# Performance work log

Measured on AMD Instinct MI355X. Metric: run time of the kernel, lower is better.

## Reference

```python
import jax, jax.numpy as jnp
import numpy as np

NUM_BANDS = 30
SPLIT_FREQ = 30
M_PARAM = 1
DIM = 2048
BATCH = 16384


def _dct_mat(N):
    # Orthonormal DCT-II matrix D: dct(x) = x @ D.T, idct(y) = y @ D
    n = np.arange(N, dtype=np.float64)
    kk = n[:, None]
    M = np.cos(np.pi * (n + 0.5) * kk / N)
    s = np.full(N, np.sqrt(2.0 / N))
    s[0] = np.sqrt(1.0 / N)
    return jnp.asarray((M * s[:, None]).astype(np.float32))


def _band_scale(freq_weights, k, N):
    # Precompute the per-frequency scale vector the torch loop applies band-by-band.
    pts = np.linspace(0, N - 1, NUM_BANDS + 1).astype(np.int64)  # torch .long() truncation
    scale = jnp.ones((N,), dtype=freq_weights.dtype)
    for i in range(NUM_BANDS):
        s, e = int(pts[i]), int(pts[i + 1])
        if e <= SPLIT_FREQ:
            f = 1.0 + freq_weights[i] * k * (1.0 - i / NUM_BANDS)
        else:
            f = 1.0 - freq_weights[i] * k * (1.0 - (i - NUM_BANDS // M_PARAM) / NUM_BANDS)
        scale = scale.at[s:e].set(f)  # bands are disjoint; base is 1
    return scale


def setup_inputs() -> dict:
    key = jax.random.key(0)
    ks = jax.random.split(key, 6)
    g = 0.02  # small init like xavier_uniform with gain 0.5
    return {
        "x": jax.random.normal(ks[0], (BATCH, DIM), dtype=jnp.float32),
        "freq_weights": jnp.ones((NUM_BANDS,), dtype=jnp.float32),
        "k": jnp.float32(0.3),
        "W1": jax.random.normal(ks[1], (1024, DIM), dtype=jnp.float32) * g,
        "b1": jnp.zeros((1024,), dtype=jnp.float32),
        "W2": jax.random.normal(ks[2], (512, 1024), dtype=jnp.float32) * g,
        "b2": jnp.zeros((512,), dtype=jnp.float32),
        "Wmu": jax.random.normal(ks[3], (256, 512), dtype=jnp.float32) * g,
        "bmu": jnp.zeros((256,), dtype=jnp.float32),
        "Wlv": jax.random.normal(ks[4], (256, 512), dtype=jnp.float32) * g,
        "blv": jnp.zeros((256,), dtype=jnp.float32),
    }


def reference(x, freq_weights, k, W1, b1, W2, b2, Wmu, bmu, Wlv, blv):
    N = x.shape[-1]
    D = _dct_mat(N)
    # DCT -> per-band reweight -> IDCT, fused as two matmuls and one vector multiply
    xd = (x @ D.T) * _band_scale(freq_weights, k, N)
    xe = xd @ D
    h = jax.nn.relu(xe @ W1.T + b1)
    h = jax.nn.relu(h @ W2.T + b2)
    mu = h @ Wmu.T + bmu
    logvar = h @ Wlv.T + blv
    return (mu, logvar)
```

## Files before the change

### kernel.cpp

```cpp
#include <hip/hip_runtime.h>
#include <hip/hip_bf16.h>
#include <math.h>

#define DIM 2048
#define BATCH 16384

typedef __attribute__((ext_vector_type(8))) short short8;
typedef __attribute__((ext_vector_type(4))) short short4v;
typedef __attribute__((ext_vector_type(4))) float floatx4;
typedef unsigned short ushort_t;

__device__ __forceinline__ ushort_t f2bf(float f) {
    union { float f; unsigned u; } v; v.f = f;
    unsigned r = v.u + 0x7FFFu + ((v.u >> 16) & 1u);
    return (ushort_t)(r >> 16);
}

__global__ void k_scale(const float* __restrict__ fw, const float* __restrict__ kp,
                        float* __restrict__ s) {
    int n = blockIdx.x * blockDim.x + threadIdx.x;
    if (n >= DIM) return;
    float kv = kp[0];
    float f = 1.0f;
    for (int i = 0; i < 30; ++i) {
        long s0 = (long)((double)i       * (double)(DIM - 1) / 30.0);
        long e0 = (long)((double)(i + 1) * (double)(DIM - 1) / 30.0);
        if (n >= s0 && n < e0) {
            if (e0 <= 30)
                f = 1.0f + fw[i] * kv * (1.0f - (float)i / 30.0f);
            else
                f = 1.0f - fw[i] * kv * (1.0f - (float)(i - 30) / 30.0f);
        }
    }
    s[n] = f;
}

__global__ void k_gen_d(ushort_t* __restrict__ D, ushort_t* __restrict__ Dt) {
    int idx = blockIdx.x * blockDim.x + threadIdx.x;
    int r = idx >> 11;
    int c = idx & (DIM - 1);
    const float w  = 7.6699039394282058e-4f;
    const float s0 = 0.02209708691207961f;
    const float s1 = 0.03125f;
    int m1 = ((2 * c + 1) * r) & (4 * DIM - 1);
    int m2 = ((2 * r + 1) * c) & (4 * DIM - 1);
    float v1 = __cosf(w * (float)m1) * (r == 0 ? s0 : s1);
    float v2 = __cosf(w * (float)m2) * (c == 0 ? s0 : s1);
    D[idx]  = f2bf(v1);
    Dt[idx] = f2bf(v2);
}

#define U_W1   262144
#define U_W2    65536
#define U_WH    16384
__global__ void k_cast_w(const float* __restrict__ W1, const float* __restrict__ W2,
                         const float* __restrict__ Wmu, const float* __restrict__ Wlv,
                         ushort_t* __restrict__ W1bf, ushort_t* __restrict__ W2bf,
                         ushort_t* __restrict__ Wcat) {
    int i = blockIdx.x * blockDim.x + threadIdx.x;
    const float* src; ushort_t* dst; int u;
    if (i < U_W1)                    { src = W1;  dst = W1bf;             u = i; }
    else if (i < U_W1 + U_W2)        { src = W2;  dst = W2bf;             u = i - U_W1; }
    else if (i < U_W1 + U_W2 + U_WH) { src = Wmu; dst = Wcat;             u = i - U_W1 - U_W2; }
    else                             { src = Wlv; dst = Wcat + 8 * U_WH;  u = i - U_W1 - U_W2 - U_WH; }
    const float4* p = reinterpret_cast<const float4*>(src) + 2 * (size_t)u;
    float4 a = p[0], b = p[1];
    short8 r;
    r[0] = (short)f2bf(a.x); r[1] = (short)f2bf(a.y);
    r[2] = (short)f2bf(a.z); r[3] = (short)f2bf(a.w);
    r[4] = (short)f2bf(b.x); r[5] = (short)f2bf(b.y);
    r[6] = (short)f2bf(b.z); r[7] = (short)f2bf(b.w);
    *reinterpret_cast<short8*>(dst + 8 * (size_t)u) = r;
}

__global__ void k_cast_x(const float* __restrict__ in, ushort_t* __restrict__ out) {
    int i = blockIdx.x * blockDim.x + threadIdx.x;
    const float4* p = reinterpret_cast<const float4*>(in) + 2 * (size_t)i;
    float4 a = p[0], b = p[1];
    short8 r;
    r[0] = (short)f2bf(a.x); r[1] = (short)f2bf(a.y);
    r[2] = (short)f2bf(a.z); r[3] = (short)f2bf(a.w);
    r[4] = (short)f2bf(b.x); r[5] = (short)f2bf(b.y);
    r[6] = (short)f2bf(b.z); r[7] = (short)f2bf(b.w);
    *reinterpret_cast<short8*>(out + 8 * (size_t)i) = r;
}

__global__ void k_red(const float* __restrict__ P, ushort_t* __restrict__ out,
                      const float* __restrict__ scale, int n4, int n4row) {
    int i = blockIdx.x * blockDim.x + threadIdx.x;
    const float4* p = reinterpret_cast<const float4*>(P);
    float4 a = p[i], b = p[i + n4], c = p[i + 2 * n4], d = p[i + 3 * n4];
    float4 s;
    s.x = a.x + b.x + c.x + d.x;
    s.y = a.y + b.y + c.y + d.y;
    s.z = a.z + b.z + c.z + d.z;
    s.w = a.w + b.w + c.w + d.w;
    if (scale) {
        float4 sc = reinterpret_cast<const float4*>(scale)[i & (n4row - 1)];
        s.x *= sc.x; s.y *= sc.y; s.z *= sc.z; s.w *= sc.w;
    }
    short4v o;
    o[0] = (short)f2bf(s.x); o[1] = (short)f2bf(s.y);
    o[2] = (short)f2bf(s.z); o[3] = (short)f2bf(s.w);
    *reinterpret_cast<short4v*>(out + 4 * (size_t)i) = o;
}

template<int TM, int TN, int BK, int EPI, bool SK4>
__device__ __forceinline__ void gemm_core(
        const ushort_t* __restrict__ A, const ushort_t* __restrict__ B,
        ushort_t* __restrict__ Cb, float* __restrict__ Cf,
        const float* __restrict__ ep0, const float* __restrict__ ep1,
        int M, int N, int K, int KC) {
    constexpr int BM = 32 * TM;
    constexpr int BN = 32 * TN;
    constexpr int SEGS = BK / 8;
    constexpr int RSH  = (BK == 32) ? 1 : 0;
    constexpr int SSH  = (SEGS == 4) ? 2 : 3;
    __shared__ __align__(16) ushort_t As[BM * BK];
    __shared__ __align__(16) ushort_t Bs[BN * BK];

    const int tid  = threadIdx.x;
    const int lane = tid & 63;
    const int wave = tid >> 6;
    const int wm   = wave >> 1;
    const int wn   = wave & 1;
    const int q    = lane >> 4;
    const int l16  = lane & 15;

    const int tilesM = M / BM;
    const int tilesN = N / BN;
    int bid = (int)blockIdx.x;
    int sk = 0;
    if constexpr (SK4) { int nt = tilesM * tilesN; sk = bid / nt; bid = bid % nt; }
    const int xcd = bid & 7;
    const int j   = bid >> 3;
    const int bm  = xcd * (tilesM >> 3) + j / tilesN;
    const int bn  = j % tilesN;

    floatx4 acc[TM][TN];
    #pragma unroll
    for (int i = 0; i < TM; ++i)
        #pragma unroll
        for (int jj = 0; jj < TN; ++jj)
            acc[i][jj] = (floatx4){0.f, 0.f, 0.f, 0.f};

    const long aBase = (long)bm * BM * K + (long)sk * KC;
    const long bBase = (long)bn * BN * K + (long)sk * KC;
    const int  KLOOP = SK4 ? KC : K;

    for (int kt = 0; kt < KLOOP; kt += BK) {
        __syncthreads();
        #pragma unroll
        for (int i = 0; i < BM * BK / 2048; ++i) {
            int idx = tid + i * 256;
            int row = idx >> SSH, seg = idx & (SEGS - 1);
            int gseg = seg ^ ((row >> RSH) & (SEGS - 1));
            const ushort_t* g = A + aBase + (long)row * K + kt + gseg * 8;
            __builtin_amdgcn_global_load_lds(
                (const __attribute__((address_space(1))) void*)g,
                (__attribute__((address_space(3))) void*)(As + idx * 8),
                16, 0, 0);
        }
        #pragma unroll
        for (int i = 0; i < BN * BK / 2048; ++i) {
            int idx = tid + i * 256;
            int row = idx >> SSH, seg = idx & (SEGS - 1);
            int gseg = seg ^ ((row >> RSH) & (SEGS - 1));
            const ushort_t* g = B + bBase + (long)row * K + kt + gseg * 8;
            __builtin_amdgcn_global_load_lds(
                (const __attribute__((address_space(1))) void*)g,
                (__attribute__((address_space(3))) void*)(Bs + idx * 8),
                16, 0, 0);
        }
        __syncthreads();

        #pragma unroll
        for (int ks = 0; ks < BK / 32; ++ks) {
            short8 af[TM], bfr[TN];
            #pragma unroll
            for (int t = 0; t < TM; ++t) {
                int srow = wm * TM * 16 + t * 16 + l16;
                int rseg = (ks * 4 + q) ^ ((srow >> RSH) & (SEGS - 1));
                af[t] = *reinterpret_cast<const short8*>(&As[srow * BK + rseg * 8]);
            }
            #pragma unroll
            for (int t = 0; t < TN; ++t) {
                int srow = wn * TN * 16 + t * 16 + l16;
                int rseg = (ks * 4 + q) ^ ((srow >> RSH) & (SEGS - 1));
                bfr[t] = *reinterpret_cast<const short8*>(&Bs[srow * BK + rseg * 8]);
            }
            #pragma unroll
            for (int i = 0; i < TM; ++i)
                #pragma unroll
                for (int jj = 0; jj < TN; ++jj)
                    acc[i][jj] = __builtin_amdgcn_mfma_f32_16x16x32_bf16(
                        af[i], bfr[jj], acc[i][jj], 0, 0, 0);
        }
    }

    #pragma unroll
    for (int i = 0; i < TM; ++i) {
        #pragma unroll
        for (int jj = 0; jj < TN; ++jj) {
            #pragma unroll
            for (int r = 0; r < 4; ++r) {
                int row = bm * BM + wm * TM * 16 + i * 16 + q * 4 + r;
                int col = bn * BN + wn * TN * 16 + jj * 16 + l16;
                float v = acc[i][jj][r];
                if constexpr (EPI == 0) {
                    Cb[(long)row * N + col] = f2bf(v * ep0[col]);
                } else if constexpr (EPI == 1) {
                    Cb[(long)row * N + col] = f2bf(v);
                } else if constexpr (EPI == 2) {
                    v += ep0[col];
                    v = v > 0.f ? v : 0.f;
                    Cb[(long)row * N + col] = f2bf(v);
                } else if constexpr (EPI == 3) {
                    const int half = N >> 1;
                    if (col < half)
                        Cf[(long)row * half + col] = v + ep0[col];
                    else
                        Cf[(long)M * half + (long)row * half + (col - half)] = v + ep1[col - half];
                } else {
                    Cf[(long)sk * M * N + (long)row * N + col] = v;
                }
            }
        }
    }
}

__global__ __launch_bounds__(256) void g0p_sk(const ushort_t* A, const ushort_t* B,
        float* P, int M, int N, int K, int KC) {
    gemm_core<4, 4, 32, 4, true>(A, B, nullptr, P, nullptr, nullptr, M, N, K, KC);
}
__global__ __launch_bounds__(256) void g1p_sk(const ushort_t* A, const ushort_t* B,
        float* P, int M, int N, int K, int KC) {
    gemm_core<4, 4, 32, 4, true>(A, B, nullptr, P, nullptr, nullptr, M, N, K, KC);
}
__global__ __launch_bounds__(256) void g2_xm1(const ushort_t* A, const ushort_t* B,
        ushort_t* Cb, const float* ep0, int M, int N, int K) {
    gemm_core<4, 4, 64, 2, false>(A, B, Cb, nullptr, ep0, nullptr, M, N, K, 0);
}
__global__ __launch_bounds__(256) void g3_h2(const ushort_t* A, const ushort_t* B,
        ushort_t* Cb, const float* ep0, int M, int N, int K) {
    gemm_core<4, 4, 32, 2, false>(A, B, Cb, nullptr, ep0, nullptr, M, N, K, 0);
}
__global__ __launch_bounds__(256) void g4_head(const ushort_t* A, const ushort_t* B,
        float* Cf, const float* ep0, const float* ep1, int M, int N, int K) {
    gemm_core<4, 4, 32, 3, false>(A, B, nullptr, Cf, ep0, ep1, M, N, K, 0);
}

extern "C" void kernel_launch(void* const* d_in, const int* in_sizes, int n_in,
                              void* d_out, int out_size, void* d_ws, size_t ws_size,
                              hipStream_t stream) {
    const float* x   = (const float*)d_in[0];
    const float* fw  = (const float*)d_in[1];
    const float* kp  = (const float*)d_in[2];
    const float* W1  = (const float*)d_in[3];
    const float* b1  = (const float*)d_in[4];
    const float* W2  = (const float*)d_in[5];
    const float* b2  = (const float*)d_in[6];
    const float* Wmu = (const float*)d_in[7];
    const float* bmu = (const float*)d_in[8];
    const float* Wlv = (const float*)d_in[9];
    const float* blv = (const float*)d_in[10];
    float* out = (float*)d_out;

    char* ws = (char*)d_ws;
    const size_t MB = 1024 * 1024;
    ushort_t* W1bf = (ushort_t*)(ws + 0);
    ushort_t* Dbf  = (ushort_t*)(ws + 4   * MB);
    ushort_t* Dtbf = (ushort_t*)(ws + 12  * MB);
    ushort_t* T1sT = (ushort_t*)(ws + 20  * MB);
    ushort_t* H1   = (ushort_t*)(ws + 0);
    float*    P    = (float*)   (ws + 32  * MB);
    ushort_t* Xbf  = (ushort_t*)(ws + 32  * MB);
    ushort_t* H2   = (ushort_t*)(ws + 96  * MB);
    ushort_t* M1T  = (ushort_t*)(ws + 112 * MB);
    ushort_t* W2bf = (ushort_t*)(ws + 116 * MB);
    ushort_t* Wcat = (ushort_t*)(ws + 117 * MB);
    float*    svec = (float*)   (ws + 118 * MB);

    hipLaunchKernelGGL(k_scale, dim3(DIM / 256), dim3(256), 0, stream, fw, kp, svec);
    hipLaunchKernelGGL(k_gen_d, dim3(DIM * DIM / 256), dim3(256), 0, stream, Dbf, Dtbf);
    hipLaunchKernelGGL(k_cast_w, dim3((U_W1 + U_W2 + 2 * U_WH) / 256), dim3(256), 0, stream,
                       W1, W2, Wmu, Wlv, W1bf, W2bf, Wcat);

    hipLaunchKernelGGL(g0p_sk, dim3(8 * 16 * 4), dim3(256), 0, stream,
                       W1bf, Dbf, P, 1024, 2048, 2048, 512);
    hipLaunchKernelGGL(k_red, dim3(1024 * 2048 / 4 / 256), dim3(256), 0, stream,
                       P, T1sT, svec, 1024 * 2048 / 4, 2048 / 4);
    hipLaunchKernelGGL(g1p_sk, dim3(8 * 16 * 4), dim3(256), 0, stream,
                       T1sT, Dtbf, P, 1024, 2048, 2048, 512);
    hipLaunchKernelGGL(k_red, dim3(1024 * 2048 / 4 / 256), dim3(256), 0, stream,
                       P, M1T, nullptr, 1024 * 2048 / 4, 2048 / 4);

    hipLaunchKernelGGL(k_cast_x, dim3(BATCH * DIM / 8 / 256), dim3(256), 0, stream, x, Xbf);

    hipLaunchKernelGGL(g2_xm1, dim3((BATCH / 128) * (1024 / 128)), dim3(256), 0, stream,
                       Xbf, M1T, H1, b1, BATCH, 1024, 2048);
    hipLaunchKernelGGL(g3_h2, dim3((BATCH / 128) * (512 / 128)), dim3(256), 0, stream,
                       H1, W2bf, H2, b2, BATCH, 512, 1024);
    hipLaunchKernelGGL(g4_head, dim3((BATCH / 128) * (512 / 128)), dim3(256), 0, stream,
                       H2, Wcat, out, bmu, blv, BATCH, 512, 512);

    (void)in_sizes; (void)n_in; (void)out_size; (void)ws_size;
}
```

Baseline: 407.7 us.

## Replace main X·M1 GEMM with 256x256 four-stage LDS-pipelined MFMA kernel

Replaces the largest GEMM (16384x1024x2048) with a dedicated kernel using 256x256 tiles, 512 threads, a 4-slot shared-memory ring filled by direct global-to-LDS loads, XOR-swizzled layout, and interleaved barriers with setprio around MFMA bursts. It also remaps block indices so each XCD works on a contiguous band of rows, to improve L2 reuse. The aim is more arithmetic intensity per tile and hiding of global load latency, traded against large LDS use (128 KB per block) and a high register count that may limit occupancy, plus hand-tuned waitcnt logic that is easy to get wrong.

Result: faster. 397.0 us (-2.6%).

```diff
diff --git a/kernel.cpp b/kernel.cpp
--- a/kernel.cpp
+++ b/kernel.cpp
@@ -229,6 +229,157 @@
     }
 }
 
+__global__ __launch_bounds__(512, 2) void g2_256(const ushort_t* __restrict__ A,
+        const ushort_t* __restrict__ B, ushort_t* __restrict__ Cb,
+        const float* __restrict__ bias, int M, int N, int K) {
+    constexpr int BM = 256, BN = 256, BK = 32;
+    __shared__ __align__(16) ushort_t As[4][BM * BK];
+    __shared__ __align__(16) ushort_t Bs[4][BN * BK];
+
+    const int tid  = threadIdx.x;
+    const int lane = tid & 63;
+    const int wave = tid >> 6;
+    const int wm   = wave >> 2;
+    const int wn   = wave & 3;
+    const int q    = lane >> 4;
+    const int l16  = lane & 15;
+
+    const int tilesM = M / BM;
+    const int tilesN = N / BN;
+    int bid = (int)blockIdx.x;
+    const int xcd = bid & 7;
+    const int jb  = bid >> 3;
+    const int bm  = xcd * (tilesM >> 3) + jb / tilesN;
+    const int bn  = jb % tilesN;
+    const int NT  = K / BK;
+
+    const long aBase = (long)bm * BM * K;
+    const long bBase = (long)bn * BN * K;
+
+    floatx4 acc[8][4];
+    #pragma unroll
+    for (int i = 0; i < 8; ++i)
+        #pragma unroll
+        for (int j = 0; j < 4; ++j)
+            acc[i][j] = (floatx4){0.f, 0.f, 0.f, 0.f};
+
+#define STAGE_A(t) do { int _sl = (t) & 3;                                          \
+        _Pragma("unroll")                                                           \
+        for (int _g = 0; _g < 2; ++_g) {                                            \
+            int _idx = _g * 512 + tid;                                              \
+            int _row = _idx >> 2, _seg = _idx & 3;                                  \
+            int _gs = _seg ^ ((_row >> 1) & 3);                                     \
+            const ushort_t* _gp = A + aBase + (long)_row * K + (t) * BK + _gs * 8;  \
+            __builtin_amdgcn_global_load_lds(                                       \
+                (const __attribute__((address_space(1))) void*)_gp,                 \
+                (__attribute__((address_space(3))) void*)(&As[_sl][_idx * 8]),      \
+                16, 0, 0);                                                          \
+        } } while (0)
+#define STAGE_B(t) do { int _sl = (t) & 3;                                          \
+        _Pragma("unroll")                                                           \
+        for (int _g = 0; _g < 2; ++_g) {                                            \
+            int _idx = _g * 512 + tid;                                              \
+            int _row = _idx >> 2, _seg = _idx & 3;                                  \
+            int _gs = _seg ^ ((_row >> 1) & 3);                                     \
+            const ushort_t* _gp = B + bBase + (long)_row * K + (t) * BK + _gs * 8;  \
+            __builtin_amdgcn_global_load_lds(                                       \
+                (const __attribute__((address_space(1))) void*)_gp,                 \
+                (__attribute__((address_space(3))) void*)(&Bs[_sl][_idx * 8]),      \
+                16, 0, 0);                                                          \
+        } } while (0)
+
+    STAGE_A(0); STAGE_B(0);
+    STAGE_A(1); STAGE_B(1);
+    STAGE_A(2); STAGE_B(2);
+    asm volatile("s_waitcnt vmcnt(8)" ::: "memory");
+    __builtin_amdgcn_s_barrier();
+    asm volatile("" ::: "memory");
+
+#define KTILE(tt, DOSTAGE, WAITOP) do {                                             \
+        const int _slot = (tt) & 3;                                                 \
+        short8 bfrag[4], afrag[4];                                                  \
+        _Pragma("unroll")                                                           \
+        for (int _j = 0; _j < 4; ++_j) {                                            \
+            int _sr = wn * 64 + _j * 16 + l16;                                      \
+            int _rs = q ^ ((_sr >> 1) & 3);                                         \
+            bfrag[_j] = *reinterpret_cast<const short8*>(&Bs[_slot][_sr * BK + _rs * 8]); \
+        }                                                                           \
+        _Pragma("unroll")                                                           \
+        for (int _i = 0; _i < 4; ++_i) {                                            \
+            int _sr = wm * 128 + _i * 16 + l16;                                     \
+            int _rs = q ^ ((_sr >> 1) & 3);                                         \
+            afrag[_i] = *reinterpret_cast<const short8*>(&As[_slot][_sr * BK + _rs * 8]); \
+        }                                                                           \
+        if (DOSTAGE) STAGE_A((tt) + 3);                                             \
+        __builtin_amdgcn_s_barrier();                                               \
+        asm volatile("s_waitcnt lgkmcnt(0)" ::: "memory");                          \
+        __builtin_amdgcn_sched_barrier(0);                                          \
+        __builtin_amdgcn_s_setprio(1);                                              \
+        _Pragma("unroll")                                                           \
+        for (int _i = 0; _i < 4; ++_i)                                              \
+            _Pragma("unroll")                                                       \
+            for (int _j = 0; _j < 4; ++_j)                                          \
+                acc[_i][_j] = __builtin_amdgcn_mfma_f32_16x16x32_bf16(              \
+                    afrag[_i], bfrag[_j], acc[_i][_j], 0, 0, 0);                    \
+        __builtin_amdgcn_s_setprio(0);                                              \
+        __builtin_amdgcn_s_barrier();                                               \
+        asm volatile("" ::: "memory");                                              \
+        short8 afrag2[4];                                                           \
+        _Pragma("unroll")                                                           \
+        for (int _i = 0; _i < 4; ++_i) {                                            \
+            int _sr = wm * 128 + 64 + _i * 16 + l16;                                \
+            int _rs = q ^ ((_sr >> 1) & 3);                                         \
+            afrag2[_i] = *reinterpret_cast<const short8*>(&As[_slot][_sr * BK + _rs * 8]); \
+        }                                                                           \
+        if (DOSTAGE) STAGE_B((tt) + 3);                                             \
+        __builtin_amdgcn_s_barrier();                                               \
+        asm volatile("s_waitcnt lgkmcnt(0)" ::: "memory");                          \
+        __builtin_amdgcn_sched_barrier(0);                                          \
+        __builtin_amdgcn_s_setprio(1);                                              \
+        _Pragma("unroll")                                                           \
+        for (int _i = 0; _i < 4; ++_i)                                              \
+            _Pragma("unroll")                                                       \
+            for (int _j = 0; _j < 4; ++_j)                                          \
+                acc[4 + _i][_j] = __builtin_amdgcn_mfma_f32_16x16x32_bf16(          \
+                    afrag2[_i], bfrag[_j], acc[4 + _i][_j], 0, 0, 0);               \
+        __builtin_amdgcn_s_setprio(0);                                              \
+        WAITOP;                                                                     \
+        __builtin_amdgcn_s_barrier();                                               \
+        asm volatile("" ::: "memory");                                              \
+    } while (0)
+
+    int t = 0;
+    for (; t < NT - 3; ++t) {
+        KTILE(t, true, asm volatile("s_waitcnt vmcnt(8)" ::: "memory"));
+    }
+    KTILE(t, false, asm volatile("s_waitcnt vmcnt(4)" ::: "memory")); ++t;
+    KTILE(t, false, asm volatile("s_waitcnt vmcnt(0)" ::: "memory")); ++t;
+    KTILE(t, false, (void)0);
+
+#undef KTILE
+#undef STAGE_A
+#undef STAGE_B
+
+    float bsv[4];
+    #pragma unroll
+    for (int j = 0; j < 4; ++j)
+        bsv[j] = bias[bn * BN + wn * 64 + j * 16 + l16];
+    #pragma unroll
+    for (int i = 0; i < 8; ++i) {
+        int row = bm * BM + wm * 128 + i * 16 + q * 4;
+        #pragma unroll
+        for (int j = 0; j < 4; ++j) {
+            int col = bn * BN + wn * 64 + j * 16 + l16;
+            #pragma unroll
+            for (int r = 0; r < 4; ++r) {
+                float v = acc[i][j][r] + bsv[j];
+                v = v > 0.f ? v : 0.f;
+                Cb[(long)(row + r) * N + col] = f2bf(v);
+            }
+        }
+    }
+}
+
 __global__ __launch_bounds__(256) void g0p_sk(const ushort_t* A, const ushort_t* B,
         float* P, int M, int N, int K, int KC) {
     gemm_core<4, 4, 32, 4, true>(A, B, nullptr, P, nullptr, nullptr, M, N, K, KC);
@@ -236,10 +387,6 @@
 __global__ __launch_bounds__(256) void g1p_sk(const ushort_t* A, const ushort_t* B,
         float* P, int M, int N, int K, int KC) {
     gemm_core<4, 4, 32, 4, true>(A, B, nullptr, P, nullptr, nullptr, M, N, K, KC);
-}
-__global__ __launch_bounds__(256) void g2_xm1(const ushort_t* A, const ushort_t* B,
-        ushort_t* Cb, const float* ep0, int M, int N, int K) {
-    gemm_core<4, 4, 64, 2, false>(A, B, Cb, nullptr, ep0, nullptr, M, N, K, 0);
 }
 __global__ __launch_bounds__(256) void g3_h2(const ushort_t* A, const ushort_t* B,
         ushort_t* Cb, const float* ep0, int M, int N, int K) {
@@ -297,7 +444,7 @@
 
     hipLaunchKernelGGL(k_cast_x, dim3(BATCH * DIM / 8 / 256), dim3(256), 0, stream, x, Xbf);
 
-    hipLaunchKernelGGL(g2_xm1, dim3((BATCH / 128) * (1024 / 128)), dim3(256), 0, stream,
+    hipLaunchKernelGGL(g2_256, dim3((BATCH / 256) * (1024 / 256)), dim3(512), 0, stream,
                        Xbf, M1T, H1, b1, BATCH, 1024, 2048);
     hipLaunchKernelGGL(g3_h2, dim3((BATCH / 128) * (512 / 128)), dim3(256), 0, stream,
                        H1, W2bf, H2, b2, BATCH, 512, 1024);
```
